# Kernel optimization log

Hardware: AMD Instinct MI355X
Metric: run time of the kernel (lower is better)

The kernel has to match this reference:

```python
import jax, jax.numpy as jnp
import numpy as np

N_AQI = 35
N_MEO = 18
H = N_AQI + 3 * N_MEO  # 89
T = 120
B = 32768


def setup_inputs() -> dict:
    key = jax.random.key(0)
    ks = jax.random.split(key, 9)
    s = 1.0 / np.sqrt(H)
    return {
        "out": jax.random.normal(ks[0], (B, T, H), dtype=jnp.float32),
        # GRUCell params (PyTorch layout: [3H, in], gate order r,z,n)
        "W_ih": jax.random.normal(ks[1], (3 * H, H), dtype=jnp.float32) * s,
        "W_hh": jax.random.normal(ks[2], (3 * H, H), dtype=jnp.float32) * s,
        "b_ih": jax.random.normal(ks[3], (3 * H,), dtype=jnp.float32) * s,
        "b_hh": jax.random.normal(ks[4], (3 * H,), dtype=jnp.float32) * s,
        # metric_fc: 89 -> 32
        "W_m": jax.random.normal(ks[5], (32, H), dtype=jnp.float32) * s,
        "b_m": jax.random.normal(ks[6], (32,), dtype=jnp.float32) * s,
        # output_fc: 32 -> 1
        "W_o": jax.random.normal(ks[7], (1, 32), dtype=jnp.float32) * (1.0 / np.sqrt(32)),
        "b_o": jax.random.normal(ks[8], (1,), dtype=jnp.float32) * (1.0 / np.sqrt(32)),
    }


def reference(out, W_ih, W_hh, b_ih, b_hh, W_m, b_m, W_o, b_o):
    h0 = jnp.zeros((out.shape[0], H), dtype=out.dtype)
    xs = jnp.transpose(out[:, :T, :], (1, 0, 2))  # (T, B, H)

    def step(h, x):
        gi = x @ W_ih.T + b_ih          # (B, 3H)
        gh = h @ W_hh.T + b_hh          # (B, 3H)
        i_r, i_z, i_n = jnp.split(gi, 3, axis=-1)
        h_r, h_z, h_n = jnp.split(gh, 3, axis=-1)
        r = jax.nn.sigmoid(i_r + h_r)
        z = jax.nn.sigmoid(i_z + h_z)
        n = jnp.tanh(i_n + r * h_n)
        h_new = (1.0 - z) * n + z * h   # PyTorch GRUCell update
        return h_new, None

    h, _ = jax.lax.scan(step, h0, xs)
    out_mmetric = jax.nn.sigmoid(h @ W_m.T + b_m)        # (B, 32)
    out_mscore = jax.nn.sigmoid(out_mmetric @ W_o.T + b_o)  # (B, 1)
    return out_mscore, out_mmetric
```

## Files before the change

kernel.cpp:

```cpp
#include <hip/hip_runtime.h>
#include <hip/hip_bf16.h>

#define Hn   89
#define Tn   120
#define BM   128
#define LDP  104
#define NTHR 768

using bf16   = __bf16;
using bf16x4 = __attribute__((ext_vector_type(4))) __bf16;
using bf16x8 = __attribute__((ext_vector_type(8))) __bf16;
typedef __attribute__((ext_vector_type(4))) float f32x4;

#define SRZ (-1.44269504f)
#define SNN ( 2.88539008f)

__device__ __forceinline__ f32x4 ld4(const float* p) {
  f32x4 v; __builtin_memcpy(&v, p, 16); return v;
}
__device__ __forceinline__ bf16x8 pack8(f32x4 a, f32x4 b) {
  bf16x8 r;
  r[0]=(bf16)a[0]; r[1]=(bf16)a[1]; r[2]=(bf16)a[2]; r[3]=(bf16)a[3];
  r[4]=(bf16)b[0]; r[5]=(bf16)b[1]; r[6]=(bf16)b[2]; r[7]=(bf16)b[3];
  return r;
}
__device__ __forceinline__ float fsig(float x) {
  return __builtin_amdgcn_rcpf(1.f + __builtin_amdgcn_exp2f(-1.44269504f * x));
}

__global__ __launch_bounds__(NTHR, 3)
void gru_fused(const float* __restrict__ X,
               const float* __restrict__ Wih,
               const float* __restrict__ Whh,
               const float* __restrict__ bih,
               const float* __restrict__ bhh,
               const float* __restrict__ Wm,
               const float* __restrict__ bm,
               const float* __restrict__ Wo,
               const float* __restrict__ bo,
               float* __restrict__ Y,
               int Bt)
{
  __shared__ __align__(16) bf16 Xl[2][BM][LDP];
  __shared__ __align__(16) bf16 Hl[2][BM][LDP];
  __shared__ float Ml[BM][32];

  const int tid  = threadIdx.x;
  const int lane = tid & 63;
  const int wv   = tid >> 6;
  const int jt   = wv >> 1;
  const int hf   = wv & 1;
  const int l15  = lane & 15;
  const int kg   = lane >> 4;
  const int jA   = jt * 16 + l15;
  const bool jAok = (jA < Hn);
  const int j0   = jt * 16 + kg * 4;
  const size_t brow0 = (size_t)blockIdx.x * BM;

  bf16x8 Bf[3][2][3];
#pragma unroll
  for (int g = 0; g < 3; ++g)
#pragma unroll
    for (int s = 0; s < 2; ++s) {
      const float* W = s ? Whh : Wih;
      const float sc = (g < 2) ? SRZ : SNN;
#pragma unroll
      for (int kt = 0; kt < 3; ++kt) {
        bf16x8 f;
        const int k0 = kt * 32 + kg * 8;
#pragma unroll
        for (int e = 0; e < 8; ++e) {
          const int k = k0 + e;
          float v = 0.f;
          if (jAok) {
            if (k < Hn) v = sc * W[(size_t)(g * Hn + jA) * Hn + k];
            else if (k == Hn && s == 0)
              v = (g < 2) ? sc * (bih[g * Hn + jA] + bhh[g * Hn + jA])
                          : sc * bih[2 * Hn + jA];
          }
          f[e] = (bf16)v;
        }
        Bf[g][s][kt] = f;
      }
    }

  float bhnq[4];
#pragma unroll
  for (int q = 0; q < 4; ++q)
    bhnq[q] = (j0 + q < Hn) ? SNN * bhh[2 * Hn + j0 + q] : 0.f;

  int soff0, soff1, loff0, loff1;
  bool lst0, lst1;
  {
    const int p0 = tid, p1 = tid + NTHR;
    const int r0 = p0 / 12, s0 = p0 - r0 * 12;
    const int r1 = p1 / 12, s1 = p1 - r1 * 12;
    lst0 = (s0 == 11); lst1 = (s1 == 11);
    soff0 = r0 * (Tn * Hn) + s0 * 8;  loff0 = r0 * LDP + s0 * 8;
    soff1 = r1 * (Tn * Hn) + s1 * 8;  loff1 = r1 * LDP + s1 * 8;
  }
  const float* Xb2 = X + brow0 * (size_t)(Tn * Hn);
  f32x4 A0, B0, A1, B1;

  auto issue = [&](int toff) {
    const float* p0 = Xb2 + soff0 + toff;
    const float* p1 = Xb2 + soff1 + toff;
    if (lst0) { f32x4 a = {p0[0], 1.0f, 0.f, 0.f}; A0 = a; B0 = (f32x4){0.f,0.f,0.f,0.f}; }
    else      { A0 = ld4(p0); B0 = ld4(p0 + 4); }
    if (lst1) { f32x4 a = {p1[0], 1.0f, 0.f, 0.f}; A1 = a; B1 = (f32x4){0.f,0.f,0.f,0.f}; }
    else      { A1 = ld4(p1); B1 = ld4(p1 + 4); }
  };
  auto commit = [&](int plane) {
    *(bf16x8*)(&Xl[plane][0][0] + loff0) = pack8(A0, B0);
    *(bf16x8*)(&Xl[plane][0][0] + loff1) = pack8(A1, B1);
  };

  float hold[4][4];
#pragma unroll
  for (int mt = 0; mt < 4; ++mt)
#pragma unroll
    for (int q = 0; q < 4; ++q) hold[mt][q] = 0.f;

  bf16*       hwb = &Hl[0][0][0] + (hf * 64 + l15) * LDP + j0;
  const bf16* xrb = &Xl[0][0][0] + (hf * 64 + l15) * LDP + kg * 8;
  const bf16* hrb = &Hl[0][0][0] + (hf * 64 + l15) * LDP + kg * 8;
  const int bufo = BM * LDP;

  issue(0);
  commit(0);
  {
    const bf16x4 z4 = {(bf16)0.f, (bf16)0.f, (bf16)0.f, (bf16)0.f};
#pragma unroll
    for (int mt = 0; mt < 4; ++mt)
      *(bf16x4*)(hwb + mt * 16 * LDP) = z4;
  }
  issue(Hn);

  int toff = 2 * Hn;
  for (int t = 0; t < Tn; ++t) {
    const int b = t & 1;
    __syncthreads();
    if (t + 1 < Tn) commit(b ^ 1);
    if (t + 2 < Tn) { issue(toff); toff += Hn; }

    __builtin_amdgcn_s_setprio(1);
    const bf16* xr = xrb + b * bufo;
    const bf16* hr = hrb + b * bufo;
    bf16*       hw = hwb + (b ^ 1) * bufo;
#pragma unroll
    for (int mt = 0; mt < 4; ++mt) {
      f32x4 ari = {0,0,0,0}, arh = {0,0,0,0};
      f32x4 azi = {0,0,0,0}, azh = {0,0,0,0};
      f32x4 ain = {0,0,0,0}, ahn = {0,0,0,0};
#pragma unroll
      for (int kt = 0; kt < 3; ++kt) {
        const bf16x8 bx = *(const bf16x8*)(xr + mt * 16 * LDP + kt * 32);
        const bf16x8 bh = *(const bf16x8*)(hr + mt * 16 * LDP + kt * 32);
        ari = __builtin_amdgcn_mfma_f32_16x16x32_bf16(Bf[0][0][kt], bx, ari, 0, 0, 0);
        arh = __builtin_amdgcn_mfma_f32_16x16x32_bf16(Bf[0][1][kt], bh, arh, 0, 0, 0);
        azi = __builtin_amdgcn_mfma_f32_16x16x32_bf16(Bf[1][0][kt], bx, azi, 0, 0, 0);
        azh = __builtin_amdgcn_mfma_f32_16x16x32_bf16(Bf[1][1][kt], bh, azh, 0, 0, 0);
        ain = __builtin_amdgcn_mfma_f32_16x16x32_bf16(Bf[2][0][kt], bx, ain, 0, 0, 0);
        ahn = __builtin_amdgcn_mfma_f32_16x16x32_bf16(Bf[2][1][kt], bh, ahn, 0, 0, 0);
      }
      bf16x4 wv4;
#pragma unroll
      for (int q = 0; q < 4; ++q) {
        const float r_ = __builtin_amdgcn_rcpf(1.f + __builtin_amdgcn_exp2f(ari[q] + arh[q]));
        const float z_ = __builtin_amdgcn_rcpf(1.f + __builtin_amdgcn_exp2f(azi[q] + azh[q]));
        const float s_ = ain[q] + r_ * (ahn[q] + bhnq[q]);
        const float n_ = fmaf(-2.f, __builtin_amdgcn_rcpf(1.f + __builtin_amdgcn_exp2f(s_)), 1.f);
        const float hv = n_ + z_ * (hold[mt][q] - n_);
        hold[mt][q] = hv;
        wv4[q] = (bf16)hv;
      }
      *(bf16x4*)(hw + mt * 16 * LDP) = wv4;
    }
    __builtin_amdgcn_s_setprio(0);
  }
  __syncthreads();

  for (int p = tid; p < BM * 32; p += NTHR) {
    const int r = p >> 5, c = p & 31;
    const bf16* hr2 = &Hl[0][r][0];
    const float* wrow = Wm + c * Hn;
    float acc = bm[c];
#pragma unroll 4
    for (int cb = 0; cb < 11; ++cb) {
      const bf16x8 hv = *(const bf16x8*)(hr2 + cb * 8);
      const f32x4 wa = ld4(wrow + cb * 8);
      const f32x4 wb = ld4(wrow + cb * 8 + 4);
      acc = fmaf((float)hv[0], wa[0], acc); acc = fmaf((float)hv[1], wa[1], acc);
      acc = fmaf((float)hv[2], wa[2], acc); acc = fmaf((float)hv[3], wa[3], acc);
      acc = fmaf((float)hv[4], wb[0], acc); acc = fmaf((float)hv[5], wb[1], acc);
      acc = fmaf((float)hv[6], wb[2], acc); acc = fmaf((float)hv[7], wb[3], acc);
    }
    acc = fmaf((float)hr2[88], wrow[88], acc);
    const float mv = fsig(acc);
    Ml[r][c] = mv;
    Y[(size_t)Bt + (brow0 + r) * 32 + c] = mv;
  }
  __syncthreads();
  if (tid < BM) {
    float acc = bo[0];
#pragma unroll
    for (int c = 0; c < 32; ++c) acc = fmaf(Ml[tid][c], Wo[c], acc);
    Y[brow0 + tid] = fsig(acc);
  }
}

extern "C" void kernel_launch(void* const* d_in, const int* in_sizes, int n_in,
                              void* d_out, int out_size, void* d_ws, size_t ws_size,
                              hipStream_t stream) {
  const float* X   = (const float*)d_in[0];
  const float* Wih = (const float*)d_in[1];
  const float* Whh = (const float*)d_in[2];
  const float* bih = (const float*)d_in[3];
  const float* bhh = (const float*)d_in[4];
  const float* Wm  = (const float*)d_in[5];
  const float* bm  = (const float*)d_in[6];
  const float* Wo  = (const float*)d_in[7];
  const float* bo  = (const float*)d_in[8];

  const int B = in_sizes[0] / (Tn * Hn);
  dim3 grid(B / BM), block(NTHR);
  gru_fused<<<grid, block, 0, stream>>>(X, Wih, Whh, bih, bhh, Wm, bm, Wo, bo,
                                        (float*)d_out, B);
}
```

Baseline: 612.2 us.

## Warp-specialize GRU with async global-to-LDS loads and smaller batch tiles

Halves the batch tile to 64 rows and uses 512 threads. Six waves handle the MFMA gate math and two producer waves stream raw fp32 X tiles into LDS with global_load_lds, so per-thread register staging and bf16 packing on the load path go away. The input-hidden and hidden-hidden MFMAs for r and z now accumulate into one accumulator. The bias is moved into the hidden operand via a constant 1.0 column, and h_old is re-read from LDS instead of being held in registers. The cost is fp32 LDS reads with packing inside the compute loop, a larger LDS footprint, and a producer-side vmcnt(0) wait every step that could stall the barrier.

```diff
diff --git a/kernel.cpp b/kernel.cpp
--- a/kernel.cpp
+++ b/kernel.cpp
@@ -1,19 +1,28 @@
 #include <hip/hip_runtime.h>
 #include <hip/hip_bf16.h>
 
-#define Hn   89
-#define Tn   120
-#define BM   128
-#define LDP  104
-#define NTHR 768
+#define Hn    89
+#define Tn    120
+#define BM    64
+#define XPF   100
+#define XPB   (XPF*4)
+#define XPLANE (BM*XPB)
+#define HPB   208
+#define HPLANE (BM*HPB)
+#define ROWB  (Tn*Hn*4)
+#define TSTEP (Hn*4)
+#define OMAX  ((unsigned)(BM*ROWB - 16))
+
+#define SRZ (-1.44269504f)
+#define SNN ( 2.88539008f)
 
 using bf16   = __bf16;
 using bf16x4 = __attribute__((ext_vector_type(4))) __bf16;
 using bf16x8 = __attribute__((ext_vector_type(8))) __bf16;
 typedef __attribute__((ext_vector_type(4))) float f32x4;
 
-#define SRZ (-1.44269504f)
-#define SNN ( 2.88539008f)
+typedef const __attribute__((address_space(1))) unsigned int guint;
+typedef __attribute__((address_space(3))) unsigned int luint;
 
 __device__ __forceinline__ f32x4 ld4(const float* p) {
   f32x4 v; __builtin_memcpy(&v, p, 16); return v;
@@ -24,11 +33,11 @@
   r[4]=(bf16)b[0]; r[5]=(bf16)b[1]; r[6]=(bf16)b[2]; r[7]=(bf16)b[3];
   return r;
 }
-__device__ __forceinline__ float fsig(float x) {
-  return __builtin_amdgcn_rcpf(1.f + __builtin_amdgcn_exp2f(-1.44269504f * x));
-}
-
-__global__ __launch_bounds__(NTHR, 3)
+__device__ __forceinline__ float frcp(float x) { return __builtin_amdgcn_rcpf(x); }
+__device__ __forceinline__ float fex2(float x) { return __builtin_amdgcn_exp2f(x); }
+__device__ __forceinline__ float fsig(float x) { return frcp(1.f + fex2(-1.44269504f * x)); }
+
+__global__ __launch_bounds__(512, 4)
 void gru_fused(const float* __restrict__ X,
                const float* __restrict__ Wih,
                const float* __restrict__ Whh,
@@ -41,170 +50,175 @@
                float* __restrict__ Y,
                int Bt)
 {
-  __shared__ __align__(16) bf16 Xl[2][BM][LDP];
-  __shared__ __align__(16) bf16 Hl[2][BM][LDP];
-  __shared__ float Ml[BM][32];
+  __shared__ __align__(16) char lds[2 * XPLANE + 2 * HPLANE];
+  char* const XF0 = lds;
+  char* const HL0 = lds + 2 * XPLANE;
 
   const int tid  = threadIdx.x;
   const int lane = tid & 63;
   const int wv   = tid >> 6;
-  const int jt   = wv >> 1;
-  const int hf   = wv & 1;
   const int l15  = lane & 15;
   const int kg   = lane >> 4;
-  const int jA   = jt * 16 + l15;
-  const bool jAok = (jA < Hn);
-  const int j0   = jt * 16 + kg * 4;
+  const bool cmp = (wv < 6);
   const size_t brow0 = (size_t)blockIdx.x * BM;
+  const char* xgw = (const char*)(X + brow0 * (size_t)(Tn * Hn));
 
   bf16x8 Bf[3][2][3];
-#pragma unroll
-  for (int g = 0; g < 3; ++g)
-#pragma unroll
-    for (int s = 0; s < 2; ++s) {
-      const float* W = s ? Whh : Wih;
-      const float sc = (g < 2) ? SRZ : SNN;
-#pragma unroll
-      for (int kt = 0; kt < 3; ++kt) {
-        bf16x8 f;
-        const int k0 = kt * 32 + kg * 8;
-#pragma unroll
-        for (int e = 0; e < 8; ++e) {
-          const int k = k0 + e;
-          float v = 0.f;
-          if (jAok) {
-            if (k < Hn) v = sc * W[(size_t)(g * Hn + jA) * Hn + k];
-            else if (k == Hn && s == 0)
-              v = (g < 2) ? sc * (bih[g * Hn + jA] + bhh[g * Hn + jA])
-                          : sc * bih[2 * Hn + jA];
+  float binq[4] = {0.f, 0.f, 0.f, 0.f};
+  if (cmp) {
+    const int jA = wv * 16 + l15;
+    const bool jAok = (jA < Hn);
+#pragma unroll
+    for (int g = 0; g < 3; ++g)
+#pragma unroll
+      for (int s = 0; s < 2; ++s) {
+        const float* W = s ? Whh : Wih;
+        const float sc = (g < 2) ? SRZ : SNN;
+#pragma unroll
+        for (int kt = 0; kt < 3; ++kt) {
+          bf16x8 f;
+          const int k0 = kt * 32 + kg * 8;
+#pragma unroll
+          for (int e = 0; e < 8; ++e) {
+            const int k = k0 + e;
+            float v = 0.f;
+            if (jAok) {
+              if (k < Hn) v = sc * W[(size_t)(g * Hn + jA) * Hn + k];
+              else if (k == Hn && s == 1)
+                v = (g < 2) ? sc * (bih[g * Hn + jA] + bhh[g * Hn + jA])
+                            : SNN * bhh[2 * Hn + jA];
+            }
+            f[e] = (bf16)v;
           }
-          f[e] = (bf16)v;
-        }
-        Bf[g][s][kt] = f;
+          Bf[g][s][kt] = f;
+        }
       }
-    }
-
-  float bhnq[4];
-#pragma unroll
-  for (int q = 0; q < 4; ++q)
-    bhnq[q] = (j0 + q < Hn) ? SNN * bhh[2 * Hn + j0 + q] : 0.f;
-
-  int soff0, soff1, loff0, loff1;
-  bool lst0, lst1;
-  {
-    const int p0 = tid, p1 = tid + NTHR;
-    const int r0 = p0 / 12, s0 = p0 - r0 * 12;
-    const int r1 = p1 / 12, s1 = p1 - r1 * 12;
-    lst0 = (s0 == 11); lst1 = (s1 == 11);
-    soff0 = r0 * (Tn * Hn) + s0 * 8;  loff0 = r0 * LDP + s0 * 8;
-    soff1 = r1 * (Tn * Hn) + s1 * 8;  loff1 = r1 * LDP + s1 * 8;
-  }
-  const float* Xb2 = X + brow0 * (size_t)(Tn * Hn);
-  f32x4 A0, B0, A1, B1;
-
-  auto issue = [&](int toff) {
-    const float* p0 = Xb2 + soff0 + toff;
-    const float* p1 = Xb2 + soff1 + toff;
-    if (lst0) { f32x4 a = {p0[0], 1.0f, 0.f, 0.f}; A0 = a; B0 = (f32x4){0.f,0.f,0.f,0.f}; }
-    else      { A0 = ld4(p0); B0 = ld4(p0 + 4); }
-    if (lst1) { f32x4 a = {p1[0], 1.0f, 0.f, 0.f}; A1 = a; B1 = (f32x4){0.f,0.f,0.f,0.f}; }
-    else      { A1 = ld4(p1); B1 = ld4(p1 + 4); }
+#pragma unroll
+    for (int q = 0; q < 4; ++q) {
+      const int j = wv * 16 + kg * 4 + q;
+      binq[q] = (j < Hn) ? SNN * bih[2 * Hn + j] : 0.f;
+    }
+  }
+
+  const unsigned cb   = (wv == 6) ? 0u : 3328u;
+  const int     nch   = (wv == 6) ? 13 : 12;
+  const unsigned dstb = cb * 4u;
+
+  auto stage = [&](char* dst, unsigned toff) {
+    unsigned l4 = (unsigned)lane * 4u;
+    asm volatile("" : "+v"(l4));
+#pragma unroll
+    for (int m = 0; m < 13; ++m) {
+      if (m < nch) {
+        const unsigned idx4 = cb + (unsigned)(m * 256) + l4;
+        const unsigned r = idx4 / 100u;
+        const unsigned c = idx4 - r * 100u;
+        unsigned o = r * (unsigned)ROWB + (c << 2) + toff;
+        if (o > OMAX) o = OMAX;
+        __builtin_amdgcn_global_load_lds(
+            (guint*)(xgw + o), (luint*)(dst + dstb + (unsigned)(m * 1024)), 16, 0, 0);
+      }
+    }
+    asm volatile("s_waitcnt vmcnt(0)" ::: "memory");
+    if (wv == 7 && lane == 63) {
+      const float x88 = *(const float*)(xgw + 63u * (unsigned)ROWB + 352u + toff);
+      *(float*)(dst + 63 * XPB + 352) = x88;
+    }
   };
-  auto commit = [&](int plane) {
-    *(bf16x8*)(&Xl[plane][0][0] + loff0) = pack8(A0, B0);
-    *(bf16x8*)(&Xl[plane][0][0] + loff1) = pack8(A1, B1);
-  };
-
-  float hold[4][4];
-#pragma unroll
-  for (int mt = 0; mt < 4; ++mt)
-#pragma unroll
-    for (int q = 0; q < 4; ++q) hold[mt][q] = 0.f;
-
-  bf16*       hwb = &Hl[0][0][0] + (hf * 64 + l15) * LDP + j0;
-  const bf16* xrb = &Xl[0][0][0] + (hf * 64 + l15) * LDP + kg * 8;
-  const bf16* hrb = &Hl[0][0][0] + (hf * 64 + l15) * LDP + kg * 8;
-  const int bufo = BM * LDP;
-
-  issue(0);
-  commit(0);
-  {
-    const bf16x4 z4 = {(bf16)0.f, (bf16)0.f, (bf16)0.f, (bf16)0.f};
+
+  const unsigned xro = (unsigned)(l15 * XPB + kg * 32);
+  const unsigned hro = (unsigned)(l15 * HPB + kg * 16);
+  const unsigned hwo = (unsigned)(l15 * HPB + (wv * 16 + kg * 4) * 2);
+
+  if (cmp) {
+    bf16x4 z4 = {(bf16)0.f, (bf16)0.f, (bf16)0.f, (bf16)0.f};
+    if (wv == 5 && kg == 2) z4[1] = (bf16)1.0f;
 #pragma unroll
     for (int mt = 0; mt < 4; ++mt)
-      *(bf16x4*)(hwb + mt * 16 * LDP) = z4;
-  }
-  issue(Hn);
-
-  int toff = 2 * Hn;
+      *(bf16x4*)(HL0 + hwo + mt * 16 * HPB) = z4;
+  } else {
+    stage(XF0, 0);
+  }
+
+  unsigned tof = TSTEP;
   for (int t = 0; t < Tn; ++t) {
     const int b = t & 1;
     __syncthreads();
-    if (t + 1 < Tn) commit(b ^ 1);
-    if (t + 2 < Tn) { issue(toff); toff += Hn; }
-
-    __builtin_amdgcn_s_setprio(1);
-    const bf16* xr = xrb + b * bufo;
-    const bf16* hr = hrb + b * bufo;
-    bf16*       hw = hwb + (b ^ 1) * bufo;
-#pragma unroll
-    for (int mt = 0; mt < 4; ++mt) {
-      f32x4 ari = {0,0,0,0}, arh = {0,0,0,0};
-      f32x4 azi = {0,0,0,0}, azh = {0,0,0,0};
-      f32x4 ain = {0,0,0,0}, ahn = {0,0,0,0};
-#pragma unroll
-      for (int kt = 0; kt < 3; ++kt) {
-        const bf16x8 bx = *(const bf16x8*)(xr + mt * 16 * LDP + kt * 32);
-        const bf16x8 bh = *(const bf16x8*)(hr + mt * 16 * LDP + kt * 32);
-        ari = __builtin_amdgcn_mfma_f32_16x16x32_bf16(Bf[0][0][kt], bx, ari, 0, 0, 0);
-        arh = __builtin_amdgcn_mfma_f32_16x16x32_bf16(Bf[0][1][kt], bh, arh, 0, 0, 0);
-        azi = __builtin_amdgcn_mfma_f32_16x16x32_bf16(Bf[1][0][kt], bx, azi, 0, 0, 0);
-        azh = __builtin_amdgcn_mfma_f32_16x16x32_bf16(Bf[1][1][kt], bh, azh, 0, 0, 0);
-        ain = __builtin_amdgcn_mfma_f32_16x16x32_bf16(Bf[2][0][kt], bx, ain, 0, 0, 0);
-        ahn = __builtin_amdgcn_mfma_f32_16x16x32_bf16(Bf[2][1][kt], bh, ahn, 0, 0, 0);
+
+    if (cmp) {
+      __builtin_amdgcn_s_setprio(1);
+      const char* xr = XF0 + b * XPLANE + xro;
+      const char* hr = HL0 + b * HPLANE + hro;
+      const char* hp = HL0 + b * HPLANE + hwo;
+      char*       hw = HL0 + (b ^ 1) * HPLANE + hwo;
+#pragma unroll
+      for (int mt = 0; mt < 4; ++mt) {
+        f32x4 ar = {0,0,0,0}, az = {0,0,0,0}, ain = {0,0,0,0}, ahn = {0,0,0,0};
+#pragma unroll
+        for (int kt = 0; kt < 3; ++kt) {
+          const f32x4 xa = *(const f32x4*)(xr + mt * (16 * XPB) + kt * 128);
+          const f32x4 xb = *(const f32x4*)(xr + mt * (16 * XPB) + kt * 128 + 16);
+          const bf16x8 xf = pack8(xa, xb);
+          const bf16x8 hf = *(const bf16x8*)(hr + mt * (16 * HPB) + kt * 64);
+          ar  = __builtin_amdgcn_mfma_f32_16x16x32_bf16(Bf[0][0][kt], xf, ar, 0, 0, 0);
+          ar  = __builtin_amdgcn_mfma_f32_16x16x32_bf16(Bf[0][1][kt], hf, ar, 0, 0, 0);
+          az  = __builtin_amdgcn_mfma_f32_16x16x32_bf16(Bf[1][0][kt], xf, az, 0, 0, 0);
+          az  = __builtin_amdgcn_mfma_f32_16x16x32_bf16(Bf[1][1][kt], hf, az, 0, 0, 0);
+          ain = __builtin_amdgcn_mfma_f32_16x16x32_bf16(Bf[2][0][kt], xf, ain, 0, 0, 0);
+          ahn = __builtin_amdgcn_mfma_f32_16x16x32_bf16(Bf[2][1][kt], hf, ahn, 0, 0, 0);
+        }
+        const bf16x4 hp4 = *(const bf16x4*)(hp + mt * (16 * HPB));
+        bf16x4 wv4;
+#pragma unroll
+        for (int q = 0; q < 4; ++q) {
+          const float r_ = frcp(1.f + fex2(ar[q]));
+          const float z_ = frcp(1.f + fex2(az[q]));
+          const float s_ = ain[q] + binq[q] + r_ * ahn[q];
+          const float n_ = fmaf(-2.f, frcp(1.f + fex2(s_)), 1.f);
+          const float hv = n_ + z_ * ((float)hp4[q] - n_);
+          wv4[q] = (bf16)hv;
+        }
+        if (wv == 5) {
+          if (kg == 2) { wv4[1] = (bf16)1.0f; wv4[2] = (bf16)0.f; wv4[3] = (bf16)0.f; }
+          if (kg == 3) { wv4[0] = (bf16)0.f; wv4[1] = (bf16)0.f;
+                         wv4[2] = (bf16)0.f; wv4[3] = (bf16)0.f; }
+        }
+        *(bf16x4*)(hw + mt * (16 * HPB)) = wv4;
       }
-      bf16x4 wv4;
-#pragma unroll
-      for (int q = 0; q < 4; ++q) {
-        const float r_ = __builtin_amdgcn_rcpf(1.f + __builtin_amdgcn_exp2f(ari[q] + arh[q]));
-        const float z_ = __builtin_amdgcn_rcpf(1.f + __builtin_amdgcn_exp2f(azi[q] + azh[q]));
-        const float s_ = ain[q] + r_ * (ahn[q] + bhnq[q]);
-        const float n_ = fmaf(-2.f, __builtin_amdgcn_rcpf(1.f + __builtin_amdgcn_exp2f(s_)), 1.f);
-        const float hv = n_ + z_ * (hold[mt][q] - n_);
-        hold[mt][q] = hv;
-        wv4[q] = (bf16)hv;
-      }
-      *(bf16x4*)(hw + mt * 16 * LDP) = wv4;
-    }
-    __builtin_amdgcn_s_setprio(0);
+      __builtin_amdgcn_s_setprio(0);
+    } else {
+      if (t + 1 < Tn) { stage(XF0 + (b ^ 1) * XPLANE, tof); tof += TSTEP; }
+    }
   }
   __syncthreads();
 
-  for (int p = tid; p < BM * 32; p += NTHR) {
+  char* const mlb = XF0;
+  for (int p = tid; p < BM * 32; p += 512) {
     const int r = p >> 5, c = p & 31;
-    const bf16* hr2 = &Hl[0][r][0];
+    const char* hr2 = HL0 + r * HPB;
     const float* wrow = Wm + c * Hn;
     float acc = bm[c];
 #pragma unroll 4
-    for (int cb = 0; cb < 11; ++cb) {
-      const bf16x8 hv = *(const bf16x8*)(hr2 + cb * 8);
-      const f32x4 wa = ld4(wrow + cb * 8);
-      const f32x4 wb = ld4(wrow + cb * 8 + 4);
+    for (int cbk = 0; cbk < 11; ++cbk) {
+      const bf16x8 hv = *(const bf16x8*)(hr2 + cbk * 16);
+      const f32x4 wa = ld4(wrow + cbk * 8);
+      const f32x4 wb = ld4(wrow + cbk * 8 + 4);
       acc = fmaf((float)hv[0], wa[0], acc); acc = fmaf((float)hv[1], wa[1], acc);
       acc = fmaf((float)hv[2], wa[2], acc); acc = fmaf((float)hv[3], wa[3], acc);
       acc = fmaf((float)hv[4], wb[0], acc); acc = fmaf((float)hv[5], wb[1], acc);
       acc = fmaf((float)hv[6], wb[2], acc); acc = fmaf((float)hv[7], wb[3], acc);
     }
-    acc = fmaf((float)hr2[88], wrow[88], acc);
+    acc = fmaf((float)*(const bf16*)(hr2 + 176), wrow[88], acc);
     const float mv = fsig(acc);
-    Ml[r][c] = mv;
+    *(float*)(mlb + r * 128 + c * 4) = mv;
     Y[(size_t)Bt + (brow0 + r) * 32 + c] = mv;
   }
   __syncthreads();
   if (tid < BM) {
     float acc = bo[0];
 #pragma unroll
-    for (int c = 0; c < 32; ++c) acc = fmaf(Ml[tid][c], Wo[c], acc);
+    for (int c = 0; c < 32; ++c)
+      acc = fmaf(*(const float*)(mlb + tid * 128 + c * 4), Wo[c], acc);
     Y[brow0 + tid] = fsig(acc);
   }
 }
@@ -223,7 +237,7 @@
   const float* bo  = (const float*)d_in[8];
 
   const int B = in_sizes[0] / (Tn * Hn);
-  dim3 grid(B / BM), block(NTHR);
+  dim3 grid(B / BM), block(512);
   gru_fused<<<grid, block, 0, stream>>>(X, Wih, Whh, bih, bhh, Wm, bm, Wo, bo,
                                         (float*)d_out, B);
 }
```

Result: slower. 626.4 us (+2.3%).
